# Kernel optimization log

Hardware: AMD Instinct MI355X
Metric: run time of the kernel (lower is better)

Reference implementation:

```python
import jax, jax.numpy as jnp
import numpy as np

B, S, H = 16, 4096, 4096
NH, NKV, HD = 32, 8, 128
NREP = NH // NKV
EPS = 1e-5


def _rmsnorm(x, eps=EPS):
    xf = x.astype(jnp.float32)
    return (xf * jax.lax.rsqrt(jnp.mean(xf * xf, axis=-1, keepdims=True) + eps)).astype(x.dtype)


def setup_inputs() -> dict:
    key = jax.random.key(0)
    ks = jax.random.split(key, 8)
    x = jax.random.normal(ks[0], (B, 1, H), dtype=jnp.float32)
    last_pos = jax.random.randint(ks[1], (B,), 0, S)
    # rope cache: [max_seq, head_dim//2, 2] = stacked (cos, sin)
    inv_freq = 1.0 / (10000.0 ** (jnp.arange(0, HD, 2, dtype=jnp.float32) / HD))  # [HD//2]
    t = jnp.arange(S, dtype=jnp.float32)
    ang = t[:, None] * inv_freq[None, :]  # [S, HD//2]
    rope_cache = jnp.stack([jnp.cos(ang), jnp.sin(ang)], axis=-1)  # [S, HD//2, 2]
    mask = jnp.ones((B, 1, 1, S), dtype=bool)
    sc = 1.0 / np.sqrt(H)
    wqkv = jax.random.normal(ks[2], ((NH + 2 * NKV) * HD, H), dtype=jnp.float32) * sc
    o_proj_w = jax.random.normal(ks[3], (H, NH * HD), dtype=jnp.float32) * sc
    cache_k = jax.random.normal(ks[4], (B, S, NKV, HD), dtype=jnp.float32)
    cache_v = jax.random.normal(ks[5], (B, S, NKV, HD), dtype=jnp.float32)
    return {"x": x, "last_pos": last_pos, "rope_cache": rope_cache, "mask": mask,
            "wqkv": wqkv, "o_proj_w": o_proj_w, "cache_k": cache_k, "cache_v": cache_v}


def _rope_decode(x, last_pos, rope_cache):
    # x: [B, 1, nh, HD]; rope_cache: [S, HD//2, 2]; last_pos: [B]
    rc = rope_cache[last_pos]  # [B, HD//2, 2] gathered per position
    rc = rc[:, None, None, :, :]  # [B,1,1,HD//2,2]
    xs = x.astype(jnp.float32).reshape(*x.shape[:-1], HD // 2, 2)
    real = xs[..., 0] * rc[..., 0] - xs[..., 1] * rc[..., 1]
    imag = xs[..., 1] * rc[..., 0] + xs[..., 0] * rc[..., 1]
    return jnp.stack([real, imag], axis=-1).reshape(x.shape).astype(x.dtype)


def reference(x, last_pos, rope_cache, mask, wqkv, o_proj_w, cache_k, cache_v):
    bsz = x.shape[0]
    qkv = jnp.einsum('bsh,oh->bso', x, wqkv)  # [B,1,(NH+2*NKV)*HD]
    q_end = NH * HD
    k_end = q_end + NKV * HD
    q = qkv[..., :q_end].reshape(bsz, 1, NH, HD)
    k = qkv[..., q_end:k_end].reshape(bsz, 1, NKV, HD)
    v = qkv[..., k_end:].reshape(bsz, 1, NKV, HD)
    # RoPE at position last_pos (decode path: start_pos = last_pos)
    q = _rope_decode(q, last_pos, rope_cache)
    k = _rope_decode(k, last_pos, rope_cache)
    # QK RMSNorm over head_dim
    q = _rmsnorm(q)
    k = _rmsnorm(k)
    # scatter new K/V into cache at last_pos
    b_idx = jnp.arange(bsz)
    keys = cache_k.at[b_idx, last_pos].set(k[:, 0])    # [B,S,NKV,HD]
    values = cache_v.at[b_idx, last_pos].set(v[:, 0])  # [B,S,NKV,HD]
    # GQA attention without materializing repeat_interleave:
    # head h uses kv group h // NREP, so reshape heads -> [NKV, NREP]
    qg = q[:, 0].reshape(bsz, NKV, NREP, HD)
    scores = jnp.einsum('bgrd,bsgd->bgrs', qg, keys) / np.sqrt(HD)  # [B,NKV,NREP,S]
    neg = jnp.finfo(scores.dtype).min
    scores = jnp.where(mask, scores, neg)  # mask [B,1,1,S] broadcasts
    probs = jax.nn.softmax(scores.astype(jnp.float32), axis=-1).astype(q.dtype)
    out = jnp.einsum('bgrs,bsgd->bgrd', probs, values)  # [B,NKV,NREP,HD]
    out = out.reshape(bsz, 1, NH * HD)
    return jnp.einsum('bso,ho->bsh', out, o_proj_w)  # [B,1,H]
```

## Files before the change

### kernel.cpp

```cpp
#include <hip/hip_runtime.h>
#include <hip/hip_bf16.h>

#define BATCH   16
#define SEQ     4096
#define HID     4096
#define NHEADS  32
#define NKVH    8
#define HDIM    128
#define NREPS   4
#define QKV_DIM 6144
#define NSCH    16
#define SCH     256

__global__ __launch_bounds__(256) void gemv16(
    const float4* __restrict__ x4,
    const float4* __restrict__ w4,
    float* __restrict__ ypart,
    int M)
{
  const int wid  = threadIdx.x >> 6;
  const int lane = threadIdx.x & 63;
  const int mb   = M / 16;
  const int ks   = blockIdx.x / mb;
  const int rb   = blockIdx.x % mb;
  const int row0 = rb * 16 + wid * 4;
  const int k0   = ks * 512;

  float acc[16][4];
#pragma unroll
  for (int b = 0; b < 16; ++b) { acc[b][0]=0.f; acc[b][1]=0.f; acc[b][2]=0.f; acc[b][3]=0.f; }

  for (int c = 0; c < 512; c += 64) {
    const int kk = k0 + c + lane;
    const long wb = (long)row0 * 1024 + kk;
    float4 w0 = w4[wb];
    float4 w1 = w4[wb + 1024];
    float4 w2 = w4[wb + 2048];
    float4 w3 = w4[wb + 3072];
    float4 xv[16];
#pragma unroll
    for (int b = 0; b < 16; ++b) xv[b] = x4[(b << 10) + kk];
#pragma unroll
    for (int b = 0; b < 16; ++b) {
      acc[b][0] = fmaf(w0.x,xv[b].x,fmaf(w0.y,xv[b].y,fmaf(w0.z,xv[b].z,fmaf(w0.w,xv[b].w,acc[b][0]))));
      acc[b][1] = fmaf(w1.x,xv[b].x,fmaf(w1.y,xv[b].y,fmaf(w1.z,xv[b].z,fmaf(w1.w,xv[b].w,acc[b][1]))));
      acc[b][2] = fmaf(w2.x,xv[b].x,fmaf(w2.y,xv[b].y,fmaf(w2.z,xv[b].z,fmaf(w2.w,xv[b].w,acc[b][2]))));
      acc[b][3] = fmaf(w3.x,xv[b].x,fmaf(w3.y,xv[b].y,fmaf(w3.z,xv[b].z,fmaf(w3.w,xv[b].w,acc[b][3]))));
    }
  }
#pragma unroll
  for (int b = 0; b < 16; ++b) {
#pragma unroll
    for (int r = 0; r < 4; ++r) {
      float v = acc[b][r];
#pragma unroll
      for (int o = 32; o; o >>= 1) v += __shfl_xor(v, o, 64);
      if (lane == 0) ypart[((long)(ks * 16 + b)) * M + row0 + r] = v;
    }
  }
}

__global__ __launch_bounds__(64) void rope_rms(
    const float*  __restrict__ qp0,
    const float*  __restrict__ qp1,
    const int*    __restrict__ last_pos,
    const float2* __restrict__ rope2,
    float* __restrict__ proc)
{
  const int b    = blockIdx.x / 48;
  const int hh   = blockIdx.x % 48;
  const int lane = threadIdx.x;
  const int off  = b * QKV_DIM + hh * HDIM;

  float2 e0 = ((const float2*)(qp0 + off))[lane];
  float2 e1 = ((const float2*)(qp1 + off))[lane];
  float ex = e0.x + e1.x, ey = e0.y + e1.y;
  float r0 = ex, r1 = ey;
  if (hh < 40) {
    const int pos = last_pos[b];
    float2 cs = rope2[pos * 64 + lane];
    r0 = ex * cs.x - ey * cs.y;
    r1 = ey * cs.x + ex * cs.y;
    float ss = r0 * r0 + r1 * r1;
#pragma unroll
    for (int o = 32; o; o >>= 1) ss += __shfl_xor(ss, o, 64);
    float scl = rsqrtf(ss * (1.0f / 128.0f) + 1e-5f);
    r0 *= scl; r1 *= scl;
  }
  ((float2*)(proc + off))[lane] = make_float2(r0, r1);
}

__global__ __launch_bounds__(256) void attn_partial(
    const float* __restrict__ proc,
    const float* __restrict__ cache_k,
    const float* __restrict__ cache_v,
    const int*   __restrict__ last_pos,
    float* __restrict__ part_out,
    float* __restrict__ part_ml)
{
  __shared__ float sc[NREPS][SCH];
  __shared__ float ps[8][512];
  __shared__ float red[4][8];

  const int ch  = blockIdx.x & (NSCH - 1);
  const int g   = (blockIdx.x >> 4) & 7;
  const int b   = blockIdx.x >> 7;
  const int tid = threadIdx.x;
  const int pos = last_pos[b];
  const int s0  = ch * SCH;

  const float4* knewg = (const float4*)(proc + b * QKV_DIM + (NHEADS + g) * HDIM);
  const float4* vnewg = (const float4*)(proc + b * QKV_DIM + (NHEADS + NKVH + g) * HDIM);
  const float4* kg = (const float4*)(cache_k + ((long)b * SEQ * NKVH) * HDIM) + g * 32;
  const float4* vg = (const float4*)(cache_v + ((long)b * SEQ * NKVH) * HDIM) + g * 32;

  const int hw  = tid >> 5;
  const int sub = tid & 31;
  const int r   = sub >> 3;
  const int sl  = sub & 7;

  const float isq = 0.08838834764831845f;
  float4 ql[4];
#pragma unroll
  for (int t = 0; t < 4; ++t) {
    float4 q = *(const float4*)(proc + b * QKV_DIM + (g * NREPS + r) * HDIM + sl * 16 + t * 4);
    ql[t] = make_float4(q.x * isq, q.y * isq, q.z * isq, q.w * isq);
  }

  float m = -3e38f;
  for (int i = hw; i < SCH; i += 16) {
    const int sA = s0 + i, sB = s0 + i + 8;
    const float4* rowA = (sA == pos) ? knewg : (kg + (long)sA * 256);
    const float4* rowB = (sB == pos) ? knewg : (kg + (long)sB * 256);
    float4 kA0 = rowA[sl*4+0], kA1 = rowA[sl*4+1], kA2 = rowA[sl*4+2], kA3 = rowA[sl*4+3];
    float4 kB0 = rowB[sl*4+0], kB1 = rowB[sl*4+1], kB2 = rowB[sl*4+2], kB3 = rowB[sl*4+3];
    float dA = kA0.x*ql[0].x + kA0.y*ql[0].y + kA0.z*ql[0].z + kA0.w*ql[0].w
             + kA1.x*ql[1].x + kA1.y*ql[1].y + kA1.z*ql[1].z + kA1.w*ql[1].w
             + kA2.x*ql[2].x + kA2.y*ql[2].y + kA2.z*ql[2].z + kA2.w*ql[2].w
             + kA3.x*ql[3].x + kA3.y*ql[3].y + kA3.z*ql[3].z + kA3.w*ql[3].w;
    float dB = kB0.x*ql[0].x + kB0.y*ql[0].y + kB0.z*ql[0].z + kB0.w*ql[0].w
             + kB1.x*ql[1].x + kB1.y*ql[1].y + kB1.z*ql[1].z + kB1.w*ql[1].w
             + kB2.x*ql[2].x + kB2.y*ql[2].y + kB2.z*ql[2].z + kB2.w*ql[2].w
             + kB3.x*ql[3].x + kB3.y*ql[3].y + kB3.z*ql[3].z + kB3.w*ql[3].w;
    dA += __shfl_xor(dA, 1); dA += __shfl_xor(dA, 2); dA += __shfl_xor(dA, 4);
    dB += __shfl_xor(dB, 1); dB += __shfl_xor(dB, 2); dB += __shfl_xor(dB, 4);
    if (sl == 0) { sc[r][i] = dA; sc[r][i + 8] = dB; }
    m = fmaxf(m, fmaxf(dA, dB));
  }
  if (sl == 0) red[r][hw] = m;
  __syncthreads();

  float m_r[4];
#pragma unroll
  for (int r2 = 0; r2 < 4; ++r2) {
    float mm = red[r2][0];
#pragma unroll
    for (int h2 = 1; h2 < 8; ++h2) mm = fmaxf(mm, red[r2][h2]);
    m_r[r2] = mm;
  }

  float lsum[4] = {0.f, 0.f, 0.f, 0.f};
  for (int i = tid; i < SCH; i += 256) {
#pragma unroll
    for (int r2 = 0; r2 < 4; ++r2) {
      float e = __expf(sc[r2][i] - m_r[r2]);
      sc[r2][i] = e;
      lsum[r2] += e;
    }
  }
  __syncthreads();
  const int wid  = tid >> 6;
  const int lane = tid & 63;
#pragma unroll
  for (int r2 = 0; r2 < 4; ++r2) {
    float v = lsum[r2];
#pragma unroll
    for (int o = 32; o; o >>= 1) v += __shfl_xor(v, o, 64);
    if (lane == 0) red[r2][wid] = v;
  }
  __syncthreads();
  float l_r[4];
#pragma unroll
  for (int r2 = 0; r2 < 4; ++r2)
    l_r[r2] = (red[r2][0] + red[r2][1]) + (red[r2][2] + red[r2][3]);

  const int slp = tid >> 5;
  const int dq  = sub;
  float4 a0 = {0,0,0,0}, a1 = {0,0,0,0}, a2 = {0,0,0,0}, a3 = {0,0,0,0};
  for (int i = slp * 32; i < slp * 32 + 32; i += 2) {
    const int sA = s0 + i, sB = s0 + i + 1;
    const float4* rA = (sA == pos) ? vnewg : (vg + (long)sA * 256);
    const float4* rB = (sB == pos) ? vnewg : (vg + (long)sB * 256);
    float4 vA = rA[dq], vB = rB[dq];
    float p0A = sc[0][i], p1A = sc[1][i], p2A = sc[2][i], p3A = sc[3][i];
    float p0B = sc[0][i+1], p1B = sc[1][i+1], p2B = sc[2][i+1], p3B = sc[3][i+1];
    a0.x += p0A*vA.x; a0.y += p0A*vA.y; a0.z += p0A*vA.z; a0.w += p0A*vA.w;
    a1.x += p1A*vA.x; a1.y += p1A*vA.y; a1.z += p1A*vA.z; a1.w += p1A*vA.w;
    a2.x += p2A*vA.x; a2.y += p2A*vA.y; a2.z += p2A*vA.z; a2.w += p2A*vA.w;
    a3.x += p3A*vA.x; a3.y += p3A*vA.y; a3.z += p3A*vA.z; a3.w += p3A*vA.w;
    a0.x += p0B*vB.x; a0.y += p0B*vB.y; a0.z += p0B*vB.z; a0.w += p0B*vB.w;
    a1.x += p1B*vB.x; a1.y += p1B*vB.y; a1.z += p1B*vB.z; a1.w += p1B*vB.w;
    a2.x += p2B*vB.x; a2.y += p2B*vB.y; a2.z += p2B*vB.z; a2.w += p2B*vB.w;
    a3.x += p3B*vB.x; a3.y += p3B*vB.y; a3.z += p3B*vB.z; a3.w += p3B*vB.w;
  }
  *(float4*)&ps[slp][0 * 128 + dq * 4] = a0;
  *(float4*)&ps[slp][1 * 128 + dq * 4] = a1;
  *(float4*)&ps[slp][2 * 128 + dq * 4] = a2;
  *(float4*)&ps[slp][3 * 128 + dq * 4] = a3;
  __syncthreads();

  const long base = ((((long)b * NKVH + g) * NSCH + ch) * NREPS) * HDIM;
  for (int idx = tid; idx < 512; idx += 256) {
    float v = 0.f;
#pragma unroll
    for (int s2 = 0; s2 < 8; ++s2) v += ps[s2][idx];
    part_out[base + idx] = v;
  }
  if (tid < 4) {
    float mm = tid==0 ? m_r[0] : tid==1 ? m_r[1] : tid==2 ? m_r[2] : m_r[3];
    float ll = tid==0 ? l_r[0] : tid==1 ? l_r[1] : tid==2 ? l_r[2] : l_r[3];
    const long mlb = (((((long)b * NKVH + g) * NSCH + ch) * NREPS) + tid) * 2;
    part_ml[mlb]     = mm;
    part_ml[mlb + 1] = ll;
  }
}

__global__ __launch_bounds__(128) void attn_combine(
    const float* __restrict__ part_out,
    const float* __restrict__ part_ml,
    float* __restrict__ attn_out)
{
  const int r = blockIdx.x & 3;
  const int g = (blockIdx.x >> 2) & 7;
  const int b = blockIdx.x >> 5;
  const int d = threadIdx.x;

  float M = -3e38f;
#pragma unroll
  for (int c = 0; c < NSCH; ++c) {
    const long idx = ((((long)b * NKVH + g) * NSCH + c) * NREPS + r) * 2;
    M = fmaxf(M, part_ml[idx]);
  }
  float L = 0.f, o = 0.f;
#pragma unroll
  for (int c = 0; c < NSCH; ++c) {
    const long idx = ((((long)b * NKVH + g) * NSCH + c) * NREPS + r) * 2;
    const float w = __expf(part_ml[idx] - M);
    L += part_ml[idx + 1] * w;
    o += w * part_out[((((long)b * NKVH + g) * NSCH + c) * NREPS + r) * HDIM + d];
  }
  attn_out[((long)b * NHEADS + g * NREPS + r) * HDIM + d] = o / L;
}

__global__ __launch_bounds__(256) void addhalves(
    const float4* __restrict__ p0, const float4* __restrict__ p1,
    float4* __restrict__ o, int n4)
{
  int i = blockIdx.x * 256 + threadIdx.x;
  if (i < n4) {
    float4 a = p0[i], bb = p1[i];
    o[i] = make_float4(a.x+bb.x, a.y+bb.y, a.z+bb.z, a.w+bb.w);
  }
}

extern "C" void kernel_launch(void* const* d_in, const int* in_sizes, int n_in,
                              void* d_out, int out_size, void* d_ws, size_t ws_size,
                              hipStream_t stream) {
  const float* x          = (const float*)d_in[0];
  const int*   last_pos   = (const int*)  d_in[1];
  const float* rope_cache = (const float*)d_in[2];
  const float* wqkv       = (const float*)d_in[4];
  const float* o_proj_w   = (const float*)d_in[5];
  const float* cache_k    = (const float*)d_in[6];
  const float* cache_v    = (const float*)d_in[7];
  float* out = (float*)d_out;
  float* ws  = (float*)d_ws;

  float* qkv_part = ws;
  float* proc     = ws + 196608;
  float* part_out = ws + 294912;
  float* part_ml  = ws + 1343488;
  float* attn_out = ws + 1359872;
  float* out_part = ws + 1425408;

  gemv16<<<(QKV_DIM / 16) * 2, 256, 0, stream>>>(
      (const float4*)x, (const float4*)wqkv, qkv_part, QKV_DIM);
  rope_rms<<<BATCH * 48, 64, 0, stream>>>(
      qkv_part, qkv_part + BATCH * QKV_DIM, last_pos,
      (const float2*)rope_cache, proc);
  attn_partial<<<BATCH * NKVH * NSCH, 256, 0, stream>>>(
      proc, cache_k, cache_v, last_pos, part_out, part_ml);
  attn_combine<<<BATCH * NKVH * NREPS, 128, 0, stream>>>(
      part_out, part_ml, attn_out);
  gemv16<<<(HID / 16) * 2, 256, 0, stream>>>(
      (const float4*)attn_out, (const float4*)o_proj_w, out_part, HID);
  addhalves<<<(BATCH * HID / 4 + 255) / 256, 256, 0, stream>>>(
      (const float4*)out_part, (const float4*)(out_part + BATCH * HID),
      (float4*)out, BATCH * HID / 4);
}
```

Measured before the change: 224.8 us.

## Fuse RoPE/RMSNorm into attention and drop split-K in output projection

Removes the standalone rope_rms kernel. Each attention block now sums the two split-K QKV partials, applies RoPE and RMSNorm for its q/k heads, and keeps q, new k and new v in shared memory. The output projection GEMV now covers the full K dimension with 8 rows per block instead of split-K, which removes the addhalves kernel. This cuts two launches and some global round trips. The cost is that RoPE/norm work is repeated across the 16 sequence-chunk blocks, and the o-proj launch has fewer, longer blocks (512), which lowers parallelism.

```diff
diff --git a/kernel.cpp b/kernel.cpp
--- a/kernel.cpp
+++ b/kernel.cpp
@@ -12,15 +12,14 @@
 #define NSCH    16
 #define SCH     256
 
-__global__ __launch_bounds__(256) void gemv16(
+__global__ __launch_bounds__(256) void gemv_qkv(
     const float4* __restrict__ x4,
     const float4* __restrict__ w4,
-    float* __restrict__ ypart,
-    int M)
+    float* __restrict__ ypart)
 {
   const int wid  = threadIdx.x >> 6;
   const int lane = threadIdx.x & 63;
-  const int mb   = M / 16;
+  const int mb   = QKV_DIM / 16;
   const int ks   = blockIdx.x / mb;
   const int rb   = blockIdx.x % mb;
   const int row0 = rb * 16 + wid * 4;
@@ -55,52 +54,26 @@
       float v = acc[b][r];
 #pragma unroll
       for (int o = 32; o; o >>= 1) v += __shfl_xor(v, o, 64);
-      if (lane == 0) ypart[((long)(ks * 16 + b)) * M + row0 + r] = v;
-    }
-  }
-}
-
-__global__ __launch_bounds__(64) void rope_rms(
-    const float*  __restrict__ qp0,
-    const float*  __restrict__ qp1,
-    const int*    __restrict__ last_pos,
-    const float2* __restrict__ rope2,
-    float* __restrict__ proc)
-{
-  const int b    = blockIdx.x / 48;
-  const int hh   = blockIdx.x % 48;
-  const int lane = threadIdx.x;
-  const int off  = b * QKV_DIM + hh * HDIM;
-
-  float2 e0 = ((const float2*)(qp0 + off))[lane];
-  float2 e1 = ((const float2*)(qp1 + off))[lane];
-  float ex = e0.x + e1.x, ey = e0.y + e1.y;
-  float r0 = ex, r1 = ey;
-  if (hh < 40) {
-    const int pos = last_pos[b];
-    float2 cs = rope2[pos * 64 + lane];
-    r0 = ex * cs.x - ey * cs.y;
-    r1 = ey * cs.x + ex * cs.y;
-    float ss = r0 * r0 + r1 * r1;
-#pragma unroll
-    for (int o = 32; o; o >>= 1) ss += __shfl_xor(ss, o, 64);
-    float scl = rsqrtf(ss * (1.0f / 128.0f) + 1e-5f);
-    r0 *= scl; r1 *= scl;
-  }
-  ((float2*)(proc + off))[lane] = make_float2(r0, r1);
+      if (lane == 0) ypart[((long)(ks * 16 + b)) * QKV_DIM + row0 + r] = v;
+    }
+  }
 }
 
 __global__ __launch_bounds__(256) void attn_partial(
-    const float* __restrict__ proc,
+    const float* __restrict__ qkv_part,
     const float* __restrict__ cache_k,
     const float* __restrict__ cache_v,
     const int*   __restrict__ last_pos,
+    const float2* __restrict__ rope2,
     float* __restrict__ part_out,
     float* __restrict__ part_ml)
 {
   __shared__ float sc[NREPS][SCH];
   __shared__ float ps[8][512];
   __shared__ float red[4][8];
+  __shared__ float qs[4][HDIM];
+  __shared__ float kn[HDIM];
+  __shared__ float vn[HDIM];
 
   const int ch  = blockIdx.x & (NSCH - 1);
   const int g   = (blockIdx.x >> 4) & 7;
@@ -108,32 +81,68 @@
   const int tid = threadIdx.x;
   const int pos = last_pos[b];
   const int s0  = ch * SCH;
-
-  const float4* knewg = (const float4*)(proc + b * QKV_DIM + (NHEADS + g) * HDIM);
-  const float4* vnewg = (const float4*)(proc + b * QKV_DIM + (NHEADS + NKVH + g) * HDIM);
+  const float isq = 0.08838834764831845f;
+
+  const int hw  = tid >> 5;
+  const int sub = tid & 31;
+
+  if (hw < 6) {
+    int rowoff;
+    if (hw < 4)       rowoff = (g * NREPS + hw) * HDIM;
+    else if (hw == 4) rowoff = (NHEADS + g) * HDIM;
+    else              rowoff = (NHEADS + NKVH + g) * HDIM;
+    float4 e0 = *(const float4*)(qkv_part + (long)b * QKV_DIM + rowoff + sub * 4);
+    float4 e1 = *(const float4*)(qkv_part + (long)(16 + b) * QKV_DIM + rowoff + sub * 4);
+    float r0 = e0.x + e1.x, r1 = e0.y + e1.y, r2 = e0.z + e1.z, r3 = e0.w + e1.w;
+    if (hw < 5) {
+      float2 cs0 = rope2[pos * 64 + sub * 2];
+      float2 cs1 = rope2[pos * 64 + sub * 2 + 1];
+      float t0 = r0 * cs0.x - r1 * cs0.y;
+      float t1 = r1 * cs0.x + r0 * cs0.y;
+      float t2 = r2 * cs1.x - r3 * cs1.y;
+      float t3 = r3 * cs1.x + r2 * cs1.y;
+      float ss = t0*t0 + t1*t1 + t2*t2 + t3*t3;
+      ss += __shfl_xor(ss, 1);  ss += __shfl_xor(ss, 2);
+      ss += __shfl_xor(ss, 4);  ss += __shfl_xor(ss, 8);
+      ss += __shfl_xor(ss, 16);
+      float scl = rsqrtf(ss * (1.0f / 128.0f) + 1e-5f);
+      r0 = t0 * scl; r1 = t1 * scl; r2 = t2 * scl; r3 = t3 * scl;
+    }
+    if (hw < 4) {
+      float* dst = &qs[hw][sub * 4];
+      dst[0] = r0 * isq; dst[1] = r1 * isq; dst[2] = r2 * isq; dst[3] = r3 * isq;
+    } else {
+      float* dst = (hw == 4) ? &kn[sub * 4] : &vn[sub * 4];
+      dst[0] = r0; dst[1] = r1; dst[2] = r2; dst[3] = r3;
+    }
+  }
+  __syncthreads();
+
   const float4* kg = (const float4*)(cache_k + ((long)b * SEQ * NKVH) * HDIM) + g * 32;
   const float4* vg = (const float4*)(cache_v + ((long)b * SEQ * NKVH) * HDIM) + g * 32;
 
-  const int hw  = tid >> 5;
-  const int sub = tid & 31;
   const int r   = sub >> 3;
   const int sl  = sub & 7;
 
-  const float isq = 0.08838834764831845f;
   float4 ql[4];
 #pragma unroll
-  for (int t = 0; t < 4; ++t) {
-    float4 q = *(const float4*)(proc + b * QKV_DIM + (g * NREPS + r) * HDIM + sl * 16 + t * 4);
-    ql[t] = make_float4(q.x * isq, q.y * isq, q.z * isq, q.w * isq);
-  }
+  for (int t = 0; t < 4; ++t) ql[t] = *(const float4*)&qs[r][sl * 16 + t * 4];
 
   float m = -3e38f;
   for (int i = hw; i < SCH; i += 16) {
     const int sA = s0 + i, sB = s0 + i + 8;
-    const float4* rowA = (sA == pos) ? knewg : (kg + (long)sA * 256);
-    const float4* rowB = (sB == pos) ? knewg : (kg + (long)sB * 256);
+    const float4* rowA = kg + (long)sA * 256;
+    const float4* rowB = kg + (long)sB * 256;
     float4 kA0 = rowA[sl*4+0], kA1 = rowA[sl*4+1], kA2 = rowA[sl*4+2], kA3 = rowA[sl*4+3];
     float4 kB0 = rowB[sl*4+0], kB1 = rowB[sl*4+1], kB2 = rowB[sl*4+2], kB3 = rowB[sl*4+3];
+    if (sA == pos) {
+      kA0 = *(const float4*)&kn[sl*16];      kA1 = *(const float4*)&kn[sl*16+4];
+      kA2 = *(const float4*)&kn[sl*16+8];    kA3 = *(const float4*)&kn[sl*16+12];
+    }
+    if (sB == pos) {
+      kB0 = *(const float4*)&kn[sl*16];      kB1 = *(const float4*)&kn[sl*16+4];
+      kB2 = *(const float4*)&kn[sl*16+8];    kB3 = *(const float4*)&kn[sl*16+12];
+    }
     float dA = kA0.x*ql[0].x + kA0.y*ql[0].y + kA0.z*ql[0].z + kA0.w*ql[0].w
              + kA1.x*ql[1].x + kA1.y*ql[1].y + kA1.z*ql[1].z + kA1.w*ql[1].w
              + kA2.x*ql[2].x + kA2.y*ql[2].y + kA2.z*ql[2].z + kA2.w*ql[2].w
@@ -189,9 +198,10 @@
   float4 a0 = {0,0,0,0}, a1 = {0,0,0,0}, a2 = {0,0,0,0}, a3 = {0,0,0,0};
   for (int i = slp * 32; i < slp * 32 + 32; i += 2) {
     const int sA = s0 + i, sB = s0 + i + 1;
-    const float4* rA = (sA == pos) ? vnewg : (vg + (long)sA * 256);
-    const float4* rB = (sB == pos) ? vnewg : (vg + (long)sB * 256);
-    float4 vA = rA[dq], vB = rB[dq];
+    float4 vA = (vg + (long)sA * 256)[dq];
+    float4 vB = (vg + (long)sB * 256)[dq];
+    if (sA == pos) vA = *(const float4*)&vn[dq * 4];
+    if (sB == pos) vB = *(const float4*)&vn[dq * 4];
     float p0A = sc[0][i], p1A = sc[1][i], p2A = sc[2][i], p3A = sc[3][i];
     float p0B = sc[0][i+1], p1B = sc[1][i+1], p2B = sc[2][i+1], p3B = sc[3][i+1];
     a0.x += p0A*vA.x; a0.y += p0A*vA.y; a0.z += p0A*vA.z; a0.w += p0A*vA.w;
@@ -252,14 +262,42 @@
   attn_out[((long)b * NHEADS + g * NREPS + r) * HDIM + d] = o / L;
 }
 
-__global__ __launch_bounds__(256) void addhalves(
-    const float4* __restrict__ p0, const float4* __restrict__ p1,
-    float4* __restrict__ o, int n4)
+__global__ __launch_bounds__(256) void gemv_oproj(
+    const float4* __restrict__ x4,
+    const float4* __restrict__ w4,
+    float* __restrict__ out)
 {
-  int i = blockIdx.x * 256 + threadIdx.x;
-  if (i < n4) {
-    float4 a = p0[i], bb = p1[i];
-    o[i] = make_float4(a.x+bb.x, a.y+bb.y, a.z+bb.z, a.w+bb.w);
+  const int wid  = threadIdx.x >> 6;
+  const int lane = threadIdx.x & 63;
+  const int row0 = blockIdx.x * 8 + wid * 2;
+
+  float acc[16][2];
+#pragma unroll
+  for (int b = 0; b < 16; ++b) { acc[b][0] = 0.f; acc[b][1] = 0.f; }
+
+  for (int c = 0; c < 1024; c += 64) {
+    const int kk = c + lane;
+    const long wb = (long)row0 * 1024 + kk;
+    float4 w0 = w4[wb];
+    float4 w1 = w4[wb + 1024];
+    float4 xv[16];
+#pragma unroll
+    for (int b = 0; b < 16; ++b) xv[b] = x4[(b << 10) + kk];
+#pragma unroll
+    for (int b = 0; b < 16; ++b) {
+      acc[b][0] = fmaf(w0.x,xv[b].x,fmaf(w0.y,xv[b].y,fmaf(w0.z,xv[b].z,fmaf(w0.w,xv[b].w,acc[b][0]))));
+      acc[b][1] = fmaf(w1.x,xv[b].x,fmaf(w1.y,xv[b].y,fmaf(w1.z,xv[b].z,fmaf(w1.w,xv[b].w,acc[b][1]))));
+    }
+  }
+#pragma unroll
+  for (int b = 0; b < 16; ++b) {
+#pragma unroll
+    for (int r = 0; r < 2; ++r) {
+      float v = acc[b][r];
+#pragma unroll
+      for (int o = 32; o; o >>= 1) v += __shfl_xor(v, o, 64);
+      if (lane == 0) out[((long)b << 12) + row0 + r] = v;
+    }
   }
 }
 
@@ -277,24 +315,17 @@
   float* ws  = (float*)d_ws;
 
   float* qkv_part = ws;
-  float* proc     = ws + 196608;
-  float* part_out = ws + 294912;
-  float* part_ml  = ws + 1343488;
-  float* attn_out = ws + 1359872;
-  float* out_part = ws + 1425408;
-
-  gemv16<<<(QKV_DIM / 16) * 2, 256, 0, stream>>>(
-      (const float4*)x, (const float4*)wqkv, qkv_part, QKV_DIM);
-  rope_rms<<<BATCH * 48, 64, 0, stream>>>(
-      qkv_part, qkv_part + BATCH * QKV_DIM, last_pos,
-      (const float2*)rope_cache, proc);
+  float* part_out = ws + 196608;
+  float* part_ml  = ws + 1245184;
+  float* attn_out = ws + 1261568;
+
+  gemv_qkv<<<(QKV_DIM / 16) * 2, 256, 0, stream>>>(
+      (const float4*)x, (const float4*)wqkv, qkv_part);
   attn_partial<<<BATCH * NKVH * NSCH, 256, 0, stream>>>(
-      proc, cache_k, cache_v, last_pos, part_out, part_ml);
+      qkv_part, cache_k, cache_v, last_pos,
+      (const float2*)rope_cache, part_out, part_ml);
   attn_combine<<<BATCH * NKVH * NREPS, 128, 0, stream>>>(
       part_out, part_ml, attn_out);
-  gemv16<<<(HID / 16) * 2, 256, 0, stream>>>(
-      (const float4*)attn_out, (const float4*)o_proj_w, out_part, HID);
-  addhalves<<<(BATCH * HID / 4 + 255) / 256, 256, 0, stream>>>(
-      (const float4*)out_part, (const float4*)(out_part + BATCH * HID),
-      (float4*)out, BATCH * HID / 4);
-}
+  gemv_oproj<<<HID / 8, 256, 0, stream>>>(
+      (const float4*)attn_out, (const float4*)o_proj_w, out);
+}
```

New measurement: 302.2 us. 34.4% more time.

## Stage KV cache through LDS with async double-buffered loads; fuse o_proj reduction

Applied to the files above, without the earlier changes.

The attention partial kernel now streams K and V rows into shared memory with asynchronous global-to-LDS loads, double-buffered per wave and gated by vmcnt waits, so the loads for the next tile overlap the dot products on the current one. The o_proj projection is replaced by a single-pass GEMV that reduces the full K dimension in one block and writes the output directly, removing the split-K partial buffer and the addhalves kernel. In exchange, the attention kernel uses about 32KB more LDS, which may limit occupancy, and it depends on hand-tuned wait counts. The new GEMV has fewer blocks (512), each doing longer loops.

```diff
diff --git a/kernel.cpp b/kernel.cpp
--- a/kernel.cpp
+++ b/kernel.cpp
@@ -12,6 +12,14 @@
 #define NSCH    16
 #define SCH     256
 
+__device__ __forceinline__ void gload16(float* lds, const float* g) {
+  __builtin_amdgcn_global_load_lds(
+      (const __attribute__((address_space(1))) unsigned int*)g,
+      (__attribute__((address_space(3))) unsigned int*)lds,
+      16, 0, 0);
+}
+#define WAITV(N) asm volatile("s_waitcnt vmcnt(" #N ")" ::: "memory")
+
 __global__ __launch_bounds__(256) void gemv16(
     const float4* __restrict__ x4,
     const float4* __restrict__ w4,
@@ -90,7 +98,7 @@
   ((float2*)(proc + off))[lane] = make_float2(r0, r1);
 }
 
-__global__ __launch_bounds__(256) void attn_partial(
+__global__ __launch_bounds__(256, 4) void attn_partial(
     const float* __restrict__ proc,
     const float* __restrict__ cache_k,
     const float* __restrict__ cache_v,
@@ -98,26 +106,27 @@
     float* __restrict__ part_out,
     float* __restrict__ part_ml)
 {
+  __shared__ float smem[8192];
   __shared__ float sc[NREPS][SCH];
-  __shared__ float ps[8][512];
-  __shared__ float red[4][8];
+  __shared__ float red[NREPS][8];
 
   const int ch  = blockIdx.x & (NSCH - 1);
   const int g   = (blockIdx.x >> 4) & 7;
   const int b   = blockIdx.x >> 7;
   const int tid = threadIdx.x;
-  const int pos = last_pos[b];
-  const int s0  = ch * SCH;
-
-  const float4* knewg = (const float4*)(proc + b * QKV_DIM + (NHEADS + g) * HDIM);
-  const float4* vnewg = (const float4*)(proc + b * QKV_DIM + (NHEADS + NKVH + g) * HDIM);
-  const float4* kg = (const float4*)(cache_k + ((long)b * SEQ * NKVH) * HDIM) + g * 32;
-  const float4* vg = (const float4*)(cache_v + ((long)b * SEQ * NKVH) * HDIM) + g * 32;
-
+  const int w   = tid >> 6;
   const int hw  = tid >> 5;
+  const int h   = hw & 1;
   const int sub = tid & 31;
   const int r   = sub >> 3;
   const int sl  = sub & 7;
+  const int pos = last_pos[b];
+  const int s0  = ch * SCH;
+
+  const float* kbase = cache_k + ((long)(b * SEQ) * NKVH + g) * HDIM;
+  const float* vbase = cache_v + ((long)(b * SEQ) * NKVH + g) * HDIM;
+  const float* knew  = proc + b * QKV_DIM + (NHEADS + g) * HDIM;
+  const float* vnew  = proc + b * QKV_DIM + (NHEADS + NKVH + g) * HDIM;
 
   const float isq = 0.08838834764831845f;
   float4 ql[4];
@@ -126,30 +135,61 @@
     float4 q = *(const float4*)(proc + b * QKV_DIM + (g * NREPS + r) * HDIM + sl * 16 + t * 4);
     ql[t] = make_float4(q.x * isq, q.y * isq, q.z * isq, q.w * isq);
   }
-
+  WAITV(0);
+
+#define STAGE_K(tt, bf) do {                                                 \
+    float* dst_ = &smem[((w * 2 + (bf)) * 8) * 128];                         \
+    _Pragma("unroll")                                                        \
+    for (int c_ = 0; c_ < 4; ++c_) {                                         \
+      const int s_ = s0 + (w << 6) + ((tt) << 3) + (c_ << 1) + h;            \
+      const float* src_ = (s_ == pos) ? (knew + (sub << 2))                  \
+                                      : (kbase + (long)s_ * 1024 + (sub << 2)); \
+      gload16(dst_ + (c_ << 8), src_);                                       \
+    }                                                                        \
+  } while (0)
+
+#define STAGE_V(tt, bf) do {                                                 \
+    float* dst_ = &smem[((w * 2 + (bf)) * 4) * 128];                         \
+    { const int s_ = s0 + (w << 6) + ((tt) << 1) + h;                        \
+      const float* src_ = (s_ == pos) ? (vnew + (sub << 2))                  \
+                                      : (vbase + (long)s_ * 1024 + (sub << 2)); \
+      gload16(dst_, src_); }                                                 \
+    { const int s_ = s0 + (w << 6) + 32 + ((tt) << 1) + h;                   \
+      const float* src_ = (s_ == pos) ? (vnew + (sub << 2))                  \
+                                      : (vbase + (long)s_ * 1024 + (sub << 2)); \
+      gload16(dst_ + 256, src_); }                                           \
+  } while (0)
+
+  STAGE_K(0, 0);
+  STAGE_K(1, 1);
   float m = -3e38f;
-  for (int i = hw; i < SCH; i += 16) {
-    const int sA = s0 + i, sB = s0 + i + 8;
-    const float4* rowA = (sA == pos) ? knewg : (kg + (long)sA * 256);
-    const float4* rowB = (sB == pos) ? knewg : (kg + (long)sB * 256);
-    float4 kA0 = rowA[sl*4+0], kA1 = rowA[sl*4+1], kA2 = rowA[sl*4+2], kA3 = rowA[sl*4+3];
-    float4 kB0 = rowB[sl*4+0], kB1 = rowB[sl*4+1], kB2 = rowB[sl*4+2], kB3 = rowB[sl*4+3];
-    float dA = kA0.x*ql[0].x + kA0.y*ql[0].y + kA0.z*ql[0].z + kA0.w*ql[0].w
-             + kA1.x*ql[1].x + kA1.y*ql[1].y + kA1.z*ql[1].z + kA1.w*ql[1].w
-             + kA2.x*ql[2].x + kA2.y*ql[2].y + kA2.z*ql[2].z + kA2.w*ql[2].w
-             + kA3.x*ql[3].x + kA3.y*ql[3].y + kA3.z*ql[3].z + kA3.w*ql[3].w;
-    float dB = kB0.x*ql[0].x + kB0.y*ql[0].y + kB0.z*ql[0].z + kB0.w*ql[0].w
-             + kB1.x*ql[1].x + kB1.y*ql[1].y + kB1.z*ql[1].z + kB1.w*ql[1].w
-             + kB2.x*ql[2].x + kB2.y*ql[2].y + kB2.z*ql[2].z + kB2.w*ql[2].w
-             + kB3.x*ql[3].x + kB3.y*ql[3].y + kB3.z*ql[3].z + kB3.w*ql[3].w;
-    dA += __shfl_xor(dA, 1); dA += __shfl_xor(dA, 2); dA += __shfl_xor(dA, 4);
-    dB += __shfl_xor(dB, 1); dB += __shfl_xor(dB, 2); dB += __shfl_xor(dB, 4);
-    if (sl == 0) { sc[r][i] = dA; sc[r][i + 8] = dB; }
-    m = fmaxf(m, fmaxf(dA, dB));
+  for (int tt = 0; tt < 8; ++tt) {
+    if (tt < 7) WAITV(4); else WAITV(0);
+    const float* kb = &smem[((w * 2 + (tt & 1)) * 8) * 128];
+#pragma unroll
+    for (int pp = 0; pp < 4; ++pp) {
+      const int p = (pp << 1) + h;
+      const float4 k0 = *(const float4*)&kb[p * 128 + sl * 16];
+      const float4 k1 = *(const float4*)&kb[p * 128 + sl * 16 + 4];
+      const float4 k2 = *(const float4*)&kb[p * 128 + sl * 16 + 8];
+      const float4 k3 = *(const float4*)&kb[p * 128 + sl * 16 + 12];
+      float d = k0.x*ql[0].x + k0.y*ql[0].y + k0.z*ql[0].z + k0.w*ql[0].w
+              + k1.x*ql[1].x + k1.y*ql[1].y + k1.z*ql[1].z + k1.w*ql[1].w
+              + k2.x*ql[2].x + k2.y*ql[2].y + k2.z*ql[2].z + k2.w*ql[2].w
+              + k3.x*ql[3].x + k3.y*ql[3].y + k3.z*ql[3].z + k3.w*ql[3].w;
+      d += __shfl_xor(d, 1); d += __shfl_xor(d, 2); d += __shfl_xor(d, 4);
+      const int i = (w << 6) + (tt << 3) + p;
+      if (sl == 0) sc[r][i] = d;
+      m = fmaxf(m, d);
+    }
+    if (tt < 6) STAGE_K(tt + 2, tt & 1);
   }
   if (sl == 0) red[r][hw] = m;
   __syncthreads();
 
+  STAGE_V(0, 0);
+  STAGE_V(1, 1);
+
   float m_r[4];
 #pragma unroll
   for (int r2 = 0; r2 < 4; ++r2) {
@@ -159,13 +199,14 @@
     m_r[r2] = mm;
   }
 
-  float lsum[4] = {0.f, 0.f, 0.f, 0.f};
-  for (int i = tid; i < SCH; i += 256) {
+  float lsum[4];
+  {
+    const int i = tid;
 #pragma unroll
     for (int r2 = 0; r2 < 4; ++r2) {
       float e = __expf(sc[r2][i] - m_r[r2]);
       sc[r2][i] = e;
-      lsum[r2] += e;
+      lsum[r2] = e;
     }
   }
   __syncthreads();
@@ -184,36 +225,35 @@
   for (int r2 = 0; r2 < 4; ++r2)
     l_r[r2] = (red[r2][0] + red[r2][1]) + (red[r2][2] + red[r2][3]);
 
-  const int slp = tid >> 5;
-  const int dq  = sub;
+  float* ps = &smem[4096];
+  const int dq = sub;
   float4 a0 = {0,0,0,0}, a1 = {0,0,0,0}, a2 = {0,0,0,0}, a3 = {0,0,0,0};
-  for (int i = slp * 32; i < slp * 32 + 32; i += 2) {
-    const int sA = s0 + i, sB = s0 + i + 1;
-    const float4* rA = (sA == pos) ? vnewg : (vg + (long)sA * 256);
-    const float4* rB = (sB == pos) ? vnewg : (vg + (long)sB * 256);
-    float4 vA = rA[dq], vB = rB[dq];
-    float p0A = sc[0][i], p1A = sc[1][i], p2A = sc[2][i], p3A = sc[3][i];
-    float p0B = sc[0][i+1], p1B = sc[1][i+1], p2B = sc[2][i+1], p3B = sc[3][i+1];
-    a0.x += p0A*vA.x; a0.y += p0A*vA.y; a0.z += p0A*vA.z; a0.w += p0A*vA.w;
-    a1.x += p1A*vA.x; a1.y += p1A*vA.y; a1.z += p1A*vA.z; a1.w += p1A*vA.w;
-    a2.x += p2A*vA.x; a2.y += p2A*vA.y; a2.z += p2A*vA.z; a2.w += p2A*vA.w;
-    a3.x += p3A*vA.x; a3.y += p3A*vA.y; a3.z += p3A*vA.z; a3.w += p3A*vA.w;
-    a0.x += p0B*vB.x; a0.y += p0B*vB.y; a0.z += p0B*vB.z; a0.w += p0B*vB.w;
-    a1.x += p1B*vB.x; a1.y += p1B*vB.y; a1.z += p1B*vB.z; a1.w += p1B*vB.w;
-    a2.x += p2B*vB.x; a2.y += p2B*vB.y; a2.z += p2B*vB.z; a2.w += p2B*vB.w;
-    a3.x += p3B*vB.x; a3.y += p3B*vB.y; a3.z += p3B*vB.z; a3.w += p3B*vB.w;
-  }
-  *(float4*)&ps[slp][0 * 128 + dq * 4] = a0;
-  *(float4*)&ps[slp][1 * 128 + dq * 4] = a1;
-  *(float4*)&ps[slp][2 * 128 + dq * 4] = a2;
-  *(float4*)&ps[slp][3 * 128 + dq * 4] = a3;
+  for (int tt = 0; tt < 16; ++tt) {
+    if (tt < 15) WAITV(2); else WAITV(0);
+    const float* vb = &smem[((w * 2 + (tt & 1)) * 4) * 128];
+#pragma unroll
+    for (int j = 0; j < 2; ++j) {
+      const int i = (w << 6) + (h << 5) + (tt << 1) + j;
+      const float4 vv = *(const float4*)&vb[(h * 2 + j) * 128 + (dq << 2)];
+      const float p0 = sc[0][i], p1 = sc[1][i], p2 = sc[2][i], p3 = sc[3][i];
+      a0.x += p0*vv.x; a0.y += p0*vv.y; a0.z += p0*vv.z; a0.w += p0*vv.w;
+      a1.x += p1*vv.x; a1.y += p1*vv.y; a1.z += p1*vv.z; a1.w += p1*vv.w;
+      a2.x += p2*vv.x; a2.y += p2*vv.y; a2.z += p2*vv.z; a2.w += p2*vv.w;
+      a3.x += p3*vv.x; a3.y += p3*vv.y; a3.z += p3*vv.z; a3.w += p3*vv.w;
+    }
+    if (tt < 14) STAGE_V(tt + 2, tt & 1);
+  }
+  *(float4*)&ps[(long)hw * 512 + 0 * 128 + (dq << 2)] = a0;
+  *(float4*)&ps[(long)hw * 512 + 1 * 128 + (dq << 2)] = a1;
+  *(float4*)&ps[(long)hw * 512 + 2 * 128 + (dq << 2)] = a2;
+  *(float4*)&ps[(long)hw * 512 + 3 * 128 + (dq << 2)] = a3;
   __syncthreads();
 
   const long base = ((((long)b * NKVH + g) * NSCH + ch) * NREPS) * HDIM;
   for (int idx = tid; idx < 512; idx += 256) {
     float v = 0.f;
 #pragma unroll
-    for (int s2 = 0; s2 < 8; ++s2) v += ps[s2][idx];
+    for (int s2 = 0; s2 < 8; ++s2) v += ps[(long)s2 * 512 + idx];
     part_out[base + idx] = v;
   }
   if (tid < 4) {
@@ -223,6 +263,8 @@
     part_ml[mlb]     = mm;
     part_ml[mlb + 1] = ll;
   }
+#undef STAGE_K
+#undef STAGE_V
 }
 
 __global__ __launch_bounds__(128) void attn_combine(
@@ -252,14 +294,42 @@
   attn_out[((long)b * NHEADS + g * NREPS + r) * HDIM + d] = o / L;
 }
 
-__global__ __launch_bounds__(256) void addhalves(
-    const float4* __restrict__ p0, const float4* __restrict__ p1,
-    float4* __restrict__ o, int n4)
-{
-  int i = blockIdx.x * 256 + threadIdx.x;
-  if (i < n4) {
-    float4 a = p0[i], bb = p1[i];
-    o[i] = make_float4(a.x+bb.x, a.y+bb.y, a.z+bb.z, a.w+bb.w);
+__global__ __launch_bounds__(256) void gemv_oproj(
+    const float4* __restrict__ x4,
+    const float4* __restrict__ w4,
+    float* __restrict__ out)
+{
+  const int wid  = threadIdx.x >> 6;
+  const int lane = threadIdx.x & 63;
+  const int row0 = blockIdx.x * 8 + wid * 2;
+
+  float acc[16][2];
+#pragma unroll
+  for (int b = 0; b < 16; ++b) { acc[b][0] = 0.f; acc[b][1] = 0.f; }
+
+  for (int c = 0; c < 1024; c += 64) {
+    const int kk = c + lane;
+    const long wb = (long)row0 * 1024 + kk;
+    float4 w0 = w4[wb];
+    float4 w1 = w4[wb + 1024];
+    float4 xv[16];
+#pragma unroll
+    for (int b = 0; b < 16; ++b) xv[b] = x4[(b << 10) + kk];
+#pragma unroll
+    for (int b = 0; b < 16; ++b) {
+      acc[b][0] = fmaf(w0.x,xv[b].x,fmaf(w0.y,xv[b].y,fmaf(w0.z,xv[b].z,fmaf(w0.w,xv[b].w,acc[b][0]))));
+      acc[b][1] = fmaf(w1.x,xv[b].x,fmaf(w1.y,xv[b].y,fmaf(w1.z,xv[b].z,fmaf(w1.w,xv[b].w,acc[b][1]))));
+    }
+  }
+#pragma unroll
+  for (int b = 0; b < 16; ++b) {
+#pragma unroll
+    for (int r = 0; r < 2; ++r) {
+      float v = acc[b][r];
+#pragma unroll
+      for (int o = 32; o; o >>= 1) v += __shfl_xor(v, o, 64);
+      if (lane == 0) out[((long)b << 12) + row0 + r] = v;
+    }
   }
 }
 
@@ -281,7 +351,6 @@
   float* part_out = ws + 294912;
   float* part_ml  = ws + 1343488;
   float* attn_out = ws + 1359872;
-  float* out_part = ws + 1425408;
 
   gemv16<<<(QKV_DIM / 16) * 2, 256, 0, stream>>>(
       (const float4*)x, (const float4*)wqkv, qkv_part, QKV_DIM);
@@ -292,9 +361,6 @@
       proc, cache_k, cache_v, last_pos, part_out, part_ml);
   attn_combine<<<BATCH * NKVH * NREPS, 128, 0, stream>>>(
       part_out, part_ml, attn_out);
-  gemv16<<<(HID / 16) * 2, 256, 0, stream>>>(
-      (const float4*)attn_out, (const float4*)o_proj_w, out_part, HID);
-  addhalves<<<(BATCH * HID / 4 + 255) / 256, 256, 0, stream>>>(
-      (const float4*)out_part, (const float4*)(out_part + BATCH * HID),
-      (float4*)out, BATCH * HID / 4);
-}
+  gemv_oproj<<<HID / 8, 256, 0, stream>>>(
+      (const float4*)attn_out, (const float4*)o_proj_w, out);
+}
```

Result: faster. 208.6 us (-7.2%).
